# Optimization experiments

Measured on AMD Instinct MI355X. Metric: run time of the kernel, lower is better.

## Reference

```python
import jax, jax.numpy as jnp
import numpy as np

DIM = 1024
B, TI, TJ = 8, 2048, 2048
EPS = 1e-5


def layernorm(x, g, b):
    mu = jnp.mean(x, axis=-1, keepdims=True)
    var = jnp.var(x, axis=-1, keepdims=True)
    return (x - mu) * jax.lax.rsqrt(var + EPS) * g + b


def setup_inputs() -> dict:
    key = jax.random.key(0)
    ks = jax.random.split(key, 12)
    s = 1.0 / np.sqrt(DIM)
    return {
        "target": jax.random.normal(ks[0], (B, TI, DIM), jnp.float32),
        "source_k": jax.random.normal(ks[1], (B, TJ, DIM), jnp.float32),
        "source_v": jax.random.normal(ks[2], (B, TJ, DIM), jnp.float32),
        "Wq": jax.random.uniform(ks[3], (DIM, DIM), jnp.float32, -s, s),
        "bq": jax.random.uniform(ks[4], (DIM,), jnp.float32, -s, s),
        "Wk": jax.random.uniform(ks[5], (DIM, DIM), jnp.float32, -s, s),
        "bk": jax.random.uniform(ks[6], (DIM,), jnp.float32, -s, s),
        "Wv": jax.random.uniform(ks[7], (DIM, DIM), jnp.float32, -s, s),
        "bv": jax.random.uniform(ks[8], (DIM,), jnp.float32, -s, s),
        "g_t": jnp.ones((DIM,), jnp.float32),
        "b_t": jnp.zeros((DIM,), jnp.float32),
        "g_k": jnp.ones((DIM,), jnp.float32),
        "b_k": jnp.zeros((DIM,), jnp.float32),
        "g_v": jnp.ones((DIM,), jnp.float32),
        "b_v": jnp.zeros((DIM,), jnp.float32),
    }


def reference(target, source_k, source_v, Wq, bq, Wk, bk, Wv, bv,
              g_t, b_t, g_k, b_k, g_v, b_v):
    scale = DIM ** (-0.5)
    t = layernorm(target, g_t, b_t)
    sk = layernorm(source_k, g_k, b_k)
    sv = layernorm(source_v, g_v, b_v)
    # torch Linear: x @ W.T + b
    q = jnp.einsum('bid,ed->bie', t, Wq) + bq
    k = jnp.einsum('bjd,ed->bje', sk, Wk) + bk
    v = jnp.einsum('bjd,ed->bje', sv, Wv) + bv
    dots = jnp.einsum('bid,bjd->bij', q, k) * scale
    attn = jax.nn.softmax(dots, axis=2)
    return jnp.einsum('bij,bjd->bid', attn, v)
```

## Files before the change

### kernel.cpp

```cpp
#include <hip/hip_runtime.h>
#include <cstdint>

using u16 = unsigned short;
using u32 = unsigned int;
typedef __attribute__((ext_vector_type(8))) short short8;
typedef __attribute__((ext_vector_type(4))) float f32x4;

__device__ __forceinline__ float bf2f(u16 u) { return __uint_as_float(((u32)u) << 16); }
__device__ __forceinline__ u16 f2bf(float f) {
    u32 u = __float_as_uint(f);
    u32 r = u + 0x7fffu + ((u >> 16) & 1u);
    return (u16)(r >> 16);
}

__device__ __forceinline__ void load_lds16(const void* g, void* l) {
    __builtin_amdgcn_global_load_lds((const __attribute__((address_space(1))) void*)g,
                                     (__attribute__((address_space(3))) void*)l, 16, 0, 0);
}

__device__ __forceinline__ void ln_row(const float* __restrict__ x,
                                       const float* __restrict__ gw,
                                       const float* __restrict__ bw,
                                       u16* __restrict__ y, int row) {
    const int tid = threadIdx.x;
    const float4 v = ((const float4*)(x + (size_t)row * 1024))[tid];
    float s  = v.x + v.y + v.z + v.w;
    float ss = v.x * v.x + v.y * v.y + v.z * v.z + v.w * v.w;
#pragma unroll
    for (int off = 32; off; off >>= 1) {
        s  += __shfl_xor(s, off);
        ss += __shfl_xor(ss, off);
    }
    __shared__ float sm[8];
    const int lane = tid & 63, wid = tid >> 6;
    if (lane == 0) { sm[wid] = s; sm[wid + 4] = ss; }
    __syncthreads();
    s  = sm[0] + sm[1] + sm[2] + sm[3];
    ss = sm[4] + sm[5] + sm[6] + sm[7];
    const float mu   = s * (1.0f / 1024.0f);
    const float var  = ss * (1.0f / 1024.0f) - mu * mu;
    const float rstd = rsqrtf(var + 1e-5f);
    const float4 g4 = ((const float4*)gw)[tid];
    const float4 b4 = ((const float4*)bw)[tid];
    u16 o[4];
    o[0] = f2bf((v.x - mu) * rstd * g4.x + b4.x);
    o[1] = f2bf((v.y - mu) * rstd * g4.y + b4.y);
    o[2] = f2bf((v.z - mu) * rstd * g4.z + b4.z);
    o[3] = f2bf((v.w - mu) * rstd * g4.w + b4.w);
    *(uint2*)(y + (size_t)row * 1024 + tid * 4) = *(uint2*)o;
}

__global__ __launch_bounds__(256)
void ln_cast_kernel(const float* __restrict__ x, const float* __restrict__ gw,
                    const float* __restrict__ bw, u16* __restrict__ y) {
    ln_row(x, gw, bw, y, blockIdx.x);
}

__global__ __launch_bounds__(256)
void ln3_kernel(const float* __restrict__ x0, const float* __restrict__ x1,
                const float* __restrict__ x2,
                const float* __restrict__ g0, const float* __restrict__ g1,
                const float* __restrict__ g2,
                const float* __restrict__ b0, const float* __restrict__ b1,
                const float* __restrict__ b2, u16* __restrict__ y) {
    const int bid = blockIdx.x;
    const int sel = bid >> 14;
    const int row = bid & 16383;
    const float* x  = (sel == 0) ? x0 : (sel == 1) ? x1 : x2;
    const float* gw = (sel == 0) ? g0 : (sel == 1) ? g1 : g2;
    const float* bw = (sel == 0) ? b0 : (sel == 1) ? b1 : b2;
    ln_row(x, gw, bw, y + ((size_t)sel << 24), row);
}

__global__ __launch_bounds__(256)
void cast3_kernel(const float* __restrict__ wa, const float* __restrict__ wb,
                  const float* __restrict__ wc, u16* __restrict__ oa) {
    const int bid = blockIdx.x;
    const int sel = bid >> 10;
    const float* s = (sel == 0) ? wa : (sel == 1) ? wb : wc;
    u16* d = oa + (size_t)sel * 1048576;
    const int i = (bid & 1023) * 256 + threadIdx.x;
    const float4 v = ((const float4*)s)[i];
    u16 o[4] = { f2bf(v.x), f2bf(v.y), f2bf(v.z), f2bf(v.w) };
    *(uint2*)(d + (size_t)i * 4) = *(uint2*)o;
}

template<int MODE>
__global__ __launch_bounds__(256, (MODE == 3 ? 3 : 4))
void gemm_bt(const u16* __restrict__ A, const u16* __restrict__ B,
             const float* __restrict__ bias0, const float* __restrict__ bias1,
             const float* __restrict__ bias2,
             void* __restrict__ Cout, void* __restrict__ Cout2,
             const int M, const int N, const int K, const float scale,
             const long sA, const long sB, const long sC)
{
    int bz, m0, n0;
    if (MODE == 2 || MODE == 3) {
        const int id = blockIdx.x;
        bz = id & 7;
        m0 = ((id >> 3) & 15) * 128;
        n0 = (id >> 7) * 128;
    } else {
        bz = (MODE == 4) ? blockIdx.z : 0;
        m0 = blockIdx.x * 128;
        n0 = blockIdx.y * 128;
    }
    A += (long)bz * sA;
    B += (long)bz * sB;
    const float* bias = (MODE == 4) ? (bz == 0 ? bias0 : bz == 1 ? bias1 : bias2)
                                    : bias0;
    __shared__ __align__(16) u16 As[128 * 64];
    __shared__ __align__(16) u16 Bs[128 * 64];
    const int tid  = threadIdx.x;
    const int lane = tid & 63, wid = tid >> 6;
    const int wm = (wid & 1) * 64, wn = (wid >> 1) * 64;

    const int scol = (tid & 7) ^ ((tid >> 3) & 7);
    const u16* ap = A + (long)(m0 + (tid >> 3)) * K + scol * 8;
    const u16* bp = B + (long)(n0 + (tid >> 3)) * K + scol * 8;
    u16* asd = As + wid * 512;
    u16* bsd = Bs + wid * 512;
    const long rs32 = 32L * K;

    f32x4 acc[4][4] = {};
    f32x4 acc_l[4] = {};
    const short8 ones8 = {16256, 16256, 16256, 16256, 16256, 16256, 16256, 16256};
    const int fr = lane & 15, fq = lane >> 4;
    const int sw = (fq ^ (fr & 7)) * 8;
    const int offA0 = (wm + fr) * 64 + sw;
    const int offA1 = offA0 ^ 32;
    const int offB0 = (wn + fr) * 64 + sw;
    const int offB1 = offB0 ^ 32;

    for (int k0 = 0; k0 < K; k0 += 64) {
#pragma unroll
        for (int rd = 0; rd < 4; rd++) {
            load_lds16(ap + k0 + rd * rs32, asd + rd * 2048);
            load_lds16(bp + k0 + rd * rs32, bsd + rd * 2048);
        }
        __syncthreads();
#pragma unroll
        for (int s = 0; s < 2; s++) {
            const int oa = s ? offA1 : offA0;
            const int ob = s ? offB1 : offB0;
            short8 b0 = *(const short8*)&Bs[ob];
            short8 b1 = *(const short8*)&Bs[ob + 1024];
            short8 b2 = *(const short8*)&Bs[ob + 2048];
            short8 b3 = *(const short8*)&Bs[ob + 3072];
#pragma unroll
            for (int i = 0; i < 4; i++) {
                const short8 a = *(const short8*)&As[oa + i * 1024];
                acc[i][0] = __builtin_amdgcn_mfma_f32_16x16x32_bf16(a, b0, acc[i][0], 0, 0, 0);
                acc[i][1] = __builtin_amdgcn_mfma_f32_16x16x32_bf16(a, b1, acc[i][1], 0, 0, 0);
                acc[i][2] = __builtin_amdgcn_mfma_f32_16x16x32_bf16(a, b2, acc[i][2], 0, 0, 0);
                acc[i][3] = __builtin_amdgcn_mfma_f32_16x16x32_bf16(a, b3, acc[i][3], 0, 0, 0);
                if (MODE == 3)
                    acc_l[i] = __builtin_amdgcn_mfma_f32_16x16x32_bf16(a, ones8, acc_l[i], 0, 0, 0);
            }
        }
        __syncthreads();
    }

    const int cn = lane & 15;
    const int cm = (lane >> 4) * 4;
    float invl[4][4];
    if (MODE == 3) {
#pragma unroll
        for (int i = 0; i < 4; i++)
#pragma unroll
            for (int r = 0; r < 4; r++) invl[i][r] = 1.0f / acc_l[i][r];
    }
#pragma unroll
    for (int i = 0; i < 4; i++) {
        const int gmb = m0 + wm + i * 16 + cm;
#pragma unroll
        for (int j = 0; j < 4; j++) {
            const int gn = n0 + wn + j * 16 + cn;
            const float bv = (MODE <= 1 || MODE == 4) ? bias[gn] : 0.0f;
            if (MODE == 1 || (MODE == 4 && bz == 2)) {
                u16* dst = (MODE == 4) ? (u16*)Cout2 : (u16*)Cout;
                const int batch = gmb >> 11;
                const int jj = gmb & 2047;
                u16 o[4];
#pragma unroll
                for (int r = 0; r < 4; r++) o[r] = f2bf(acc[i][j][r] + bv);
                *(uint2*)(dst + ((long)batch * N + gn) * 2048 + jj) = *(uint2*)o;
            } else if (MODE == 0 || MODE == 4) {
                u16* dst = (u16*)Cout + ((MODE == 4) ? (long)bz * 16777216 : 0);
#pragma unroll
                for (int r = 0; r < 4; r++)
                    dst[(long)(gmb + r) * N + gn] = f2bf(acc[i][j][r] + bv);
            } else {
#pragma unroll
                for (int r = 0; r < 4; r++) {
                    const long gm = gmb + r;
                    float v = acc[i][j][r];
                    if (MODE == 2) v = __expf(v * scale);
                    if (MODE == 3)
                        ((float*)Cout)[(long)bz * sC + gm * N + gn] = v * invl[i][r];
                    else
                        ((u16*)Cout)[(long)bz * sC + gm * N + gn] = f2bf(v);
                }
            }
        }
    }
}

__device__ __forceinline__ void ph_mid() {
    __builtin_amdgcn_sched_barrier(0);
    __builtin_amdgcn_s_barrier();
    asm volatile("s_waitcnt lgkmcnt(0)" ::: "memory");
    __builtin_amdgcn_sched_barrier(0);
}
__device__ __forceinline__ void ph_end() {
    __builtin_amdgcn_sched_barrier(0);
    __builtin_amdgcn_s_barrier();
    __builtin_amdgcn_sched_barrier(0);
}

#define RDAH(reg, mh) do { \
    aF[0] = *(const short8*)&(reg)[ offA + (mh)*8192 + 0*1024];        \
    aF[1] = *(const short8*)&(reg)[(offA + (mh)*8192 + 0*1024) ^ 32];  \
    aF[2] = *(const short8*)&(reg)[ offA + (mh)*8192 + 1*1024];        \
    aF[3] = *(const short8*)&(reg)[(offA + (mh)*8192 + 1*1024) ^ 32];  \
    aF[4] = *(const short8*)&(reg)[ offA + (mh)*8192 + 2*1024];        \
    aF[5] = *(const short8*)&(reg)[(offA + (mh)*8192 + 2*1024) ^ 32];  \
    aF[6] = *(const short8*)&(reg)[ offA + (mh)*8192 + 3*1024];        \
    aF[7] = *(const short8*)&(reg)[(offA + (mh)*8192 + 3*1024) ^ 32];  } while (0)

#define RDBH(dst, reg, nh) do { \
    dst[0] = *(const short8*)&(reg)[ offB + (nh)*8192 + 0*1024];        \
    dst[1] = *(const short8*)&(reg)[(offB + (nh)*8192 + 0*1024) ^ 32];  \
    dst[2] = *(const short8*)&(reg)[ offB + (nh)*8192 + 1*1024];        \
    dst[3] = *(const short8*)&(reg)[(offB + (nh)*8192 + 1*1024) ^ 32];  } while (0)

#define MMQ(mh, nh, bF) do { \
    __builtin_amdgcn_s_setprio(1); \
    _Pragma("unroll") \
    for (int s_ = 0; s_ < 2; s_++) { \
        _Pragma("unroll") \
        for (int i_ = 0; i_ < 4; i_++) { \
            _Pragma("unroll") \
            for (int j_ = 0; j_ < 2; j_++) \
                acc[(mh)*4+i_][(nh)*2+j_] = __builtin_amdgcn_mfma_f32_16x16x32_bf16( \
                    aF[2*i_+s_], bF[2*j_+s_], acc[(mh)*4+i_][(nh)*2+j_], 0, 0, 0); \
        } \
    } \
    __builtin_amdgcn_s_setprio(0); } while (0)

#define STA(reg, hm, kt) do { \
    const u16* s_ = apg + (hm) * rH + (long)(kt) * 64; \
    u16* d_ = (reg) + (hm) * 8192 + w * 1024; \
    load_lds16(s_, d_); \
    load_lds16(s_ + rK8, d_ + 512); } while (0)

#define STB(reg, hm, kt) do { \
    const u16* s_ = bpg + (hm) * rH + (long)(kt) * 64; \
    u16* d_ = (reg) + (hm) * 8192 + w * 1024; \
    load_lds16(s_, d_); \
    load_lds16(s_ + rK8, d_ + 512); } while (0)

template<int MODE>
__global__ __launch_bounds__(512, 1)
void gemm8(const u16* __restrict__ A, const u16* __restrict__ B,
           const float* __restrict__ bias0, const float* __restrict__ bias1,
           const float* __restrict__ bias2,
           void* __restrict__ Cout, void* __restrict__ Cout2,
           const int M, const int N, const int K, const float scale,
           const long sA, const long sB, const long sC)
{
    int bz, m0, n0;
    if (MODE == 2) {
        const int id = blockIdx.x;
        bz = id & 7;
        m0 = ((id >> 3) & 7) * 256;
        n0 = (id >> 6) * 256;
    } else {
        bz = blockIdx.z;
        m0 = blockIdx.x * 256;
        n0 = blockIdx.y * 256;
    }
    A += (long)bz * sA;
    B += (long)bz * sB;
    const float* bias = (MODE == 4) ? (bz == 0 ? bias0 : bz == 1 ? bias1 : bias2)
                                    : bias0;

    __shared__ __align__(16) u16 lds[65536];
    u16* const Ar0 = lds;
    u16* const Ar1 = lds + 16384;
    u16* const Br0 = lds + 32768;
    u16* const Br1 = lds + 49152;

    const int tid = threadIdx.x;
    const int w = tid >> 6, l = tid & 63;
    const int cgrp = (l & 7) ^ ((l >> 3) & 7);
    const long rK8 = 8L * K;
    const long rH  = 128L * K;
    const u16* apg = A + (long)(m0 + w * 16 + (l >> 3)) * K + cgrp * 8;
    const u16* bpg = B + (long)(n0 + w * 16 + (l >> 3)) * K + cgrp * 8;

    const int w1 = w & 1;
    const int wn2 = (w >> 1) * 32;
    const int fr = l & 15, fq = l >> 4;
    const int sw8 = (fq ^ (fr & 7)) * 8;
    const int offA = (w1 * 64 + fr) * 64 + sw8;
    const int offB = (wn2 + fr) * 64 + sw8;

    f32x4 acc[8][4] = {};
    short8 aF[8];
    short8 bF0[4], bF1[4];

    STB(Br0, 0, 0); STB(Br0, 1, 0); STA(Ar0, 0, 0); STA(Ar0, 1, 0);
    STB(Br1, 0, 1); STB(Br1, 1, 1); STA(Ar1, 0, 1); STA(Ar1, 1, 1);
    __builtin_amdgcn_sched_barrier(0);
    asm volatile("s_waitcnt vmcnt(8)" ::: "memory");
    __builtin_amdgcn_s_barrier();
    asm volatile("" ::: "memory");
    __builtin_amdgcn_sched_barrier(0);

    const int NI = K >> 7;
    for (int it = 0; it < NI; ++it) {
        const bool nl = (it < NI - 1);
        const int t2 = 2 * it + 2, t3 = 2 * it + 3;
        RDAH(Ar0, 0); RDBH(bF0, Br0, 0);
        ph_mid();
        MMQ(0, 0, bF0);
        ph_end();
        RDBH(bF1, Br0, 1);
        if (nl) { STB(Br0, 0, t2); STA(Ar0, 0, t2); }
        ph_mid();
        MMQ(0, 1, bF1);
        ph_end();
        RDAH(Ar0, 1);
        if (nl) STB(Br0, 1, t2);
        ph_mid();
        MMQ(1, 0, bF0);
        ph_end();
        if (nl) STA(Ar0, 1, t2);
        ph_mid();
        MMQ(1, 1, bF1);
        __builtin_amdgcn_sched_barrier(0);
        if (nl) asm volatile("s_waitcnt vmcnt(8)" ::: "memory");
        else    asm volatile("s_waitcnt vmcnt(0)" ::: "memory");
        __builtin_amdgcn_s_barrier();
        asm volatile("" ::: "memory");
        __builtin_amdgcn_sched_barrier(0);
        RDAH(Ar1, 0); RDBH(bF0, Br1, 0);
        ph_mid();
        MMQ(0, 0, bF0);
        ph_end();
        RDBH(bF1, Br1, 1);
        if (nl) { STB(Br1, 0, t3); STA(Ar1, 0, t3); }
        ph_mid();
        MMQ(0, 1, bF1);
        ph_end();
        RDAH(Ar1, 1);
        if (nl) STB(Br1, 1, t3);
        ph_mid();
        MMQ(1, 0, bF0);
        ph_end();
        if (nl) STA(Ar1, 1, t3);
        ph_mid();
        MMQ(1, 1, bF1);
        __builtin_amdgcn_sched_barrier(0);
        if (nl) asm volatile("s_waitcnt vmcnt(8)" ::: "memory");
        else    asm volatile("s_waitcnt vmcnt(0)" ::: "memory");
        __builtin_amdgcn_s_barrier();
        asm volatile("" ::: "memory");
        __builtin_amdgcn_sched_barrier(0);
    }

    const int cn = l & 15, cm = (l >> 4) * 4;
#pragma unroll
    for (int i = 0; i < 8; i++) {
        const int gmb = m0 + (i >> 2) * 128 + w1 * 64 + (i & 3) * 16 + cm;
#pragma unroll
        for (int j = 0; j < 4; j++) {
            const int gn = n0 + (j >> 1) * 128 + wn2 + (j & 1) * 16 + cn;
            if (MODE == 4) {
                const float bv = bias[gn];
                if (bz == 2) {
                    const int batch = gmb >> 11, jj = gmb & 2047;
                    u16 o[4];
#pragma unroll
                    for (int r = 0; r < 4; r++) o[r] = f2bf(acc[i][j][r] + bv);
                    *(uint2*)((u16*)Cout2 + ((long)batch * N + gn) * 2048 + jj) = *(uint2*)o;
                } else {
                    u16* dst = (u16*)Cout + (long)bz * ((long)M * N);
#pragma unroll
                    for (int r = 0; r < 4; r++)
                        dst[(long)(gmb + r) * N + gn] = f2bf(acc[i][j][r] + bv);
                }
            } else {
#pragma unroll
                for (int r = 0; r < 4; r++)
                    ((u16*)Cout)[(long)bz * sC + (long)(gmb + r) * N + gn] =
                        f2bf(__expf(acc[i][j][r] * scale));
            }
        }
    }
}

extern "C" void kernel_launch(void* const* d_in, const int* in_sizes, int n_in,
                              void* d_out, int out_size, void* d_ws, size_t ws_size,
                              hipStream_t stream) {
    const float* target = (const float*)d_in[0];
    const float* src_k  = (const float*)d_in[1];
    const float* src_v  = (const float*)d_in[2];
    const float* Wq = (const float*)d_in[3];
    const float* bq = (const float*)d_in[4];
    const float* Wk = (const float*)d_in[5];
    const float* bk = (const float*)d_in[6];
    const float* Wv = (const float*)d_in[7];
    const float* bv = (const float*)d_in[8];
    const float* g_t = (const float*)d_in[9];
    const float* b_t = (const float*)d_in[10];
    const float* g_k = (const float*)d_in[11];
    const float* b_k = (const float*)d_in[12];
    const float* g_v = (const float*)d_in[13];
    const float* b_v = (const float*)d_in[14];

    char* ws = (char*)d_ws;
    const float scale = 0.03125f;
    const size_t MB = 1048576;

    if (ws_size >= 198 * MB) {
        u16* q   = (u16*)(ws + 0);
        u16* kk  = (u16*)(ws + 32 * MB);
        u16* vT  = (u16*)(ws + 64 * MB);
        u16* ln3 = (u16*)(ws + 96 * MB);
        u16* wqb = (u16*)(ws + 192 * MB);
        u16* S   = (u16*)(ws + 96 * MB);

        cast3_kernel<<<3072, 256, 0, stream>>>(Wq, Wk, Wv, wqb);
        ln3_kernel<<<49152, 256, 0, stream>>>(target, src_k, src_v,
                                              g_t, g_k, g_v, b_t, b_k, b_v, ln3);
        gemm8<4><<<dim3(64, 4, 3), 512, 0, stream>>>(ln3, wqb, bq, bk, bv,
            q, vT, 16384, 1024, 1024, 1.0f, 16777216L, 1048576L, 0);
        gemm8<2><<<512, 512, 0, stream>>>(q, kk, nullptr, nullptr, nullptr, S, nullptr,
            2048, 2048, 1024, scale, 2048L * 1024, 2048L * 1024, 2048L * 2048);
        gemm_bt<3><<<1024, 256, 0, stream>>>(S, vT, nullptr, nullptr, nullptr, d_out, nullptr,
            2048, 1024, 2048, 1.0f, 2048L * 2048, 1024L * 2048, 2048L * 1024);
    } else {
        u16* q   = (u16*)(ws + 0);
        u16* kk  = (u16*)(ws + 32 * MB);
        u16* vT  = (u16*)(ws + 64 * MB);
        u16* ln  = (u16*)(ws + 96 * MB);
        u16* wqb = (u16*)(ws + 128 * MB);
        u16* wkb = wqb + 1048576;
        u16* wvb = wkb + 1048576;
        u16* S   = (u16*)(ws + 96 * MB);

        cast3_kernel<<<3072, 256, 0, stream>>>(Wq, Wk, Wv, wqb);
        ln_cast_kernel<<<16384, 256, 0, stream>>>(target, g_t, b_t, ln);
        gemm_bt<0><<<dim3(128, 8, 1), 256, 0, stream>>>(ln, wqb, bq, nullptr, nullptr,
            q, nullptr, 16384, 1024, 1024, 1.0f, 0, 0, 0);
        ln_cast_kernel<<<16384, 256, 0, stream>>>(src_k, g_k, b_k, ln);
        gemm_bt<0><<<dim3(128, 8, 1), 256, 0, stream>>>(ln, wkb, bk, nullptr, nullptr,
            kk, nullptr, 16384, 1024, 1024, 1.0f, 0, 0, 0);
        ln_cast_kernel<<<16384, 256, 0, stream>>>(src_v, g_v, b_v, ln);
        gemm_bt<1><<<dim3(128, 8, 1), 256, 0, stream>>>(ln, wvb, bv, nullptr, nullptr,
            vT, nullptr, 16384, 1024, 1024, 1.0f, 0, 0, 0);
        gemm_bt<2><<<2048, 256, 0, stream>>>(q, kk, nullptr, nullptr, nullptr, S, nullptr,
            2048, 2048, 1024, scale, 2048L * 1024, 2048L * 1024, 2048L * 2048);
        gemm_bt<3><<<1024, 256, 0, stream>>>(S, vT, nullptr, nullptr, nullptr, d_out, nullptr,
            2048, 1024, 2048, 1.0f, 2048L * 2048, 1024L * 2048, 2048L * 1024);
    }
}
```

Before: 496.1 us.

## Fuse softmax row sums into QK GEMM and run PV through gemm8

```diff
diff --git a/kernel.cpp b/kernel.cpp
--- a/kernel.cpp
+++ b/kernel.cpp
@@ -83,6 +83,11 @@
     const float4 v = ((const float4*)s)[i];
     u16 o[4] = { f2bf(v.x), f2bf(v.y), f2bf(v.z), f2bf(v.w) };
     *(uint2*)(d + (size_t)i * 4) = *(uint2*)o;
+}
+
+__global__ __launch_bounds__(256)
+void zerof_kernel(float* __restrict__ p) {
+    p[blockIdx.x * 256 + threadIdx.x] = 0.0f;
 }
 
 template<int MODE>
@@ -270,7 +275,7 @@
            const long sA, const long sB, const long sC)
 {
     int bz, m0, n0;
-    if (MODE == 2) {
+    if (MODE == 2 || MODE == 5) {
         const int id = blockIdx.x;
         bz = id & 7;
         m0 = ((id >> 3) & 7) * 256;
@@ -374,6 +379,13 @@
 #pragma unroll
     for (int i = 0; i < 8; i++) {
         const int gmb = m0 + (i >> 2) * 128 + w1 * 64 + (i & 3) * 16 + cm;
+        float inv[4];
+        if (MODE == 5) {
+            const float4 l4 = *(const float4*)(bias + (long)bz * 2048 + gmb);
+            inv[0] = 1.0f / l4.x; inv[1] = 1.0f / l4.y;
+            inv[2] = 1.0f / l4.z; inv[3] = 1.0f / l4.w;
+        }
+        float rs[4] = {0.0f, 0.0f, 0.0f, 0.0f};
 #pragma unroll
         for (int j = 0; j < 4; j++) {
             const int gn = n0 + (j >> 1) * 128 + wn2 + (j & 1) * 16 + cn;
@@ -391,11 +403,31 @@
                     for (int r = 0; r < 4; r++)
                         dst[(long)(gmb + r) * N + gn] = f2bf(acc[i][j][r] + bv);
                 }
+            } else if (MODE == 5) {
+#pragma unroll
+                for (int r = 0; r < 4; r++)
+                    ((float*)Cout)[(long)bz * sC + (long)(gmb + r) * N + gn] =
+                        acc[i][j][r] * inv[r];
             } else {
 #pragma unroll
-                for (int r = 0; r < 4; r++)
-                    ((u16*)Cout)[(long)bz * sC + (long)(gmb + r) * N + gn] =
-                        f2bf(__expf(acc[i][j][r] * scale));
+                for (int r = 0; r < 4; r++) {
+                    const float e = __expf(acc[i][j][r] * scale);
+                    const u16 h = f2bf(e);
+                    ((u16*)Cout)[(long)bz * sC + (long)(gmb + r) * N + gn] = h;
+                    rs[r] += bf2f(h);
+                }
+            }
+        }
+        if (MODE == 2) {
+#pragma unroll
+            for (int r = 0; r < 4; r++) {
+                float s = rs[r];
+                s += __shfl_xor(s, 1);
+                s += __shfl_xor(s, 2);
+                s += __shfl_xor(s, 4);
+                s += __shfl_xor(s, 8);
+                if (fr == 0)
+                    atomicAdd((float*)Cout2 + (long)bz * 2048 + gmb + r, s);
             }
         }
     }
@@ -431,15 +463,17 @@
         u16* ln3 = (u16*)(ws + 96 * MB);
         u16* wqb = (u16*)(ws + 192 * MB);
         u16* S   = (u16*)(ws + 96 * MB);
+        float* L = (float*)(ws + 160 * MB);
 
         cast3_kernel<<<3072, 256, 0, stream>>>(Wq, Wk, Wv, wqb);
         ln3_kernel<<<49152, 256, 0, stream>>>(target, src_k, src_v,
                                               g_t, g_k, g_v, b_t, b_k, b_v, ln3);
         gemm8<4><<<dim3(64, 4, 3), 512, 0, stream>>>(ln3, wqb, bq, bk, bv,
             q, vT, 16384, 1024, 1024, 1.0f, 16777216L, 1048576L, 0);
-        gemm8<2><<<512, 512, 0, stream>>>(q, kk, nullptr, nullptr, nullptr, S, nullptr,
+        zerof_kernel<<<64, 256, 0, stream>>>(L);
+        gemm8<2><<<512, 512, 0, stream>>>(q, kk, nullptr, nullptr, nullptr, S, L,
             2048, 2048, 1024, scale, 2048L * 1024, 2048L * 1024, 2048L * 2048);
-        gemm_bt<3><<<1024, 256, 0, stream>>>(S, vT, nullptr, nullptr, nullptr, d_out, nullptr,
+        gemm8<5><<<256, 512, 0, stream>>>(S, vT, L, nullptr, nullptr, d_out, nullptr,
             2048, 1024, 2048, 1.0f, 2048L * 2048, 1024L * 2048, 2048L * 1024);
     } else {
         u16* q   = (u16*)(ws + 0);
```

Measured after the change: 486.6 us. No clear change (-1.9%).
